# Performance work log

Hardware: AMD Instinct MI355X
Metric: run time of the kernel (lower is better)

Reference implementation:

```python
import jax, jax.numpy as jnp
import numpy as np

GROUPS = 8   # GroupNorm groups
TOP_K = 2    # top-k routing
TEMP = 1.0   # gate temperature
EPS_GN = 1e-5


def conv1d(x, w, b=None):
    # x: (B,C,T), w: (Cout,Cin,K) -> (B,Cout,T), 'same' padding
    pad = (w.shape[-1] - 1) // 2
    y = jax.lax.conv_general_dilated(x, w, (1,), [(pad, pad)],
                                     dimension_numbers=('NCH', 'OIH', 'NCH'))
    return y if b is None else y + b[None, :, None]


def group_norm(x, gamma, beta, groups=GROUPS, eps=EPS_GN):
    B, C, T = x.shape
    xg = x.reshape(B, groups, C // groups, T)
    mu = xg.mean((2, 3), keepdims=True)
    var = xg.var((2, 3), keepdims=True)
    xn = ((xg - mu) * jax.lax.rsqrt(var + eps)).reshape(B, C, T)
    return xn * gamma[None, :, None] + beta[None, :, None]


def layer_norm(x, gamma, beta, eps=EPS_GN):
    mu = x.mean(-1, keepdims=True)
    var = x.var(-1, keepdims=True)
    return (x - mu) * jax.lax.rsqrt(var + eps) * gamma + beta


def gelu(x):
    return jax.nn.gelu(x, approximate=False)  # torch nn.GELU default (erf)


def setup_inputs() -> dict:
    key = jax.random.key(0)
    ks = jax.random.split(key, 32)
    B, C, T = 32, 16, 2048
    E, CO, K = 8, 128, 5
    HID, CTX, DIN, DEMB = 128, 64, 8, 16
    GIN = CTX + DEMB
    n = lambda i, shape, s=0.05: jax.random.normal(ks[i], shape, dtype=jnp.float32) * s
    return {
        'x': jax.random.normal(ks[0], (B, C, T), dtype=jnp.float32),
        'demo': jax.random.normal(ks[1], (B, DIN), dtype=jnp.float32),
        # router context CNN (Conv1d no bias -> GroupNorm -> GELU)
        'rw': n(2, (HID, C, K)), 'rg': jnp.ones((HID,), jnp.float32), 'rb': jnp.zeros((HID,), jnp.float32),
        # router MLP: Linear -> LayerNorm -> GELU -> Linear
        'm1_w': n(3, (HID, HID)), 'm1_b': jnp.zeros((HID,), jnp.float32),
        'ln_g': jnp.ones((HID,), jnp.float32), 'ln_b': jnp.zeros((HID,), jnp.float32),
        'm2_w': n(4, (CTX, HID)), 'm2_b': jnp.zeros((CTX,), jnp.float32),
        # demographics embedder: Linear -> LayerNorm -> GELU -> Linear
        'd1_w': n(5, (2 * DEMB, DIN)), 'd1_b': jnp.zeros((2 * DEMB,), jnp.float32),
        'dln_g': jnp.ones((2 * DEMB,), jnp.float32), 'dln_b': jnp.zeros((2 * DEMB,), jnp.float32),
        'd2_w': n(6, (DEMB, 2 * DEMB)), 'd2_b': jnp.zeros((DEMB,), jnp.float32),
        # gate linear
        'g_w': n(7, (E, GIN)), 'g_b': jnp.zeros((E,), jnp.float32),
        # specialised expert CNNs (stacked over E): Conv1d -> GroupNorm -> GELU
        'ew': n(8, (E, CO, C, K)), 'eb': jnp.zeros((E, CO), jnp.float32),
        'eg': jnp.ones((E, CO), jnp.float32), 'ebt': jnp.zeros((E, CO), jnp.float32),
        # shared (always-on) expert CNN
        'sw': n(9, (CO, C, K)), 'sb': jnp.zeros((CO,), jnp.float32),
        'sg': jnp.ones((CO,), jnp.float32), 'sbt': jnp.zeros((CO,), jnp.float32),
    }


def reference(x, demo, rw, rg, rb, m1_w, m1_b, ln_g, ln_b, m2_w, m2_b,
              d1_w, d1_b, dln_g, dln_b, d2_w, d2_b, g_w, g_b,
              ew, eb, eg, ebt, sw, sb, sg, sbt):
    # ---- router: context CNN -> GAP -> MLP -> r (B, CTX)
    h = gelu(group_norm(conv1d(x, rw), rg, rb))
    r = h.mean(-1)  # GAP over time
    r = gelu(layer_norm(r @ m1_w.T + m1_b, ln_g, ln_b))
    r = r @ m2_w.T + m2_b
    # ---- demographics embedding, concat onto routing vector
    d = gelu(layer_norm(demo @ d1_w.T + d1_b, dln_g, dln_b))
    d = d @ d2_w.T + d2_b
    r = jnp.concatenate([r, d], axis=-1)  # (B, CTX+DEMB)
    # ---- gate: softmax + top-k mask + renormalise
    logits = (r @ g_w.T + g_b) / TEMP
    weights_soft = jax.nn.softmax(logits, axis=-1)  # (B, E)
    _, topk_idx = jax.lax.top_k(weights_soft, TOP_K)
    Bn = weights_soft.shape[0]
    mask = jnp.zeros_like(weights_soft).at[jnp.arange(Bn)[:, None], topk_idx].set(1.0)
    wh = weights_soft * mask
    weights_hard = wh / (wh.sum(-1, keepdims=True) + 1e-9)
    # ---- experts (dense compute, top-k-masked combine) + shared expert
    expert = lambda w, b, g, be: gelu(group_norm(conv1d(x, w, b), g, be))
    eo = jax.vmap(expert)(ew, eb, eg, ebt)  # (E, B, CO, T)
    shared = gelu(group_norm(conv1d(x, sw, sb), sg, sbt))  # (B, CO, T)
    out = shared + jnp.einsum('be,ebct->bct', weights_hard, eo)
    return out
```

## Files before the change

kernel.cpp:

```cpp
#include <hip/hip_runtime.h>
#include <math.h>

#define B_    32
#define CIN   16
#define T_    2048
#define NG    8
#define CPG   16
#define HID   128
#define KW    5
#define EPS_  1e-5f

#define NROW  2080
#define ROWS  16

#define SH_EWF  1064960
#define SH_RWF  1175552
#define FO_R0   593920
#define FO_GW   598016
#define FO_GI   598080

typedef float f32x4 __attribute__((ext_vector_type(4)));
typedef short s16x8 __attribute__((ext_vector_type(8)));

__device__ __forceinline__ float gelu_fast(float y) {
    float p = y * y;
    float u = y * (0.7978845608028654f + 0.03567740813636141f * p);
    float au = fabsf(u);
    float e = __expf(2.0f * au);
    float th = copysignf(1.0f - 2.0f * __builtin_amdgcn_rcpf(e + 1.0f), u);
    return 0.5f * y * (1.0f + th);
}

__device__ __forceinline__ float gelu_erf(float y) {
    return 0.5f * y * (1.0f + erff(y * 0.70710678118654752440f));
}

__device__ __forceinline__ short bf16r(float f) {
    unsigned u = __builtin_bit_cast(unsigned, f);
    u = u + 0x7FFFu + ((u >> 16) & 1u);
    return (short)(u >> 16);
}

__global__ __launch_bounds__(256) void transpose_kernel(
    const float* __restrict__ x, short* __restrict__ xt)
{
    const int b = blockIdx.x, half = blockIdx.y;
    const int tid = threadIdx.x;
    const float* xb = x + (size_t)b * CIN * T_;
    short* xtb = xt + (size_t)b * NROW * ROWS;
    const int t0 = (half * 256 + tid) * 4;

    float v[CIN][4];
    #pragma unroll
    for (int ci = 0; ci < CIN; ++ci)
        *(f32x4*)v[ci] = *(const f32x4*)(xb + ci * T_ + t0);

    #pragma unroll
    for (int tt = 0; tt < 4; ++tt) {
        s16x8 lo, hi;
        #pragma unroll
        for (int ci = 0; ci < 8; ++ci) lo[ci] = bf16r(v[ci][tt]);
        #pragma unroll
        for (int ci = 0; ci < 8; ++ci) hi[ci] = bf16r(v[ci + 8][tt]);
        short* rp = xtb + (size_t)(t0 + tt + 2) * ROWS;
        *(s16x8*)rp = lo;
        *(s16x8*)(rp + 8) = hi;
    }
    if (half == 0 && tid < 32) {
        int r = (tid < 2) ? tid : 2048 + tid;
        s16x8 z = {0, 0, 0, 0, 0, 0, 0, 0};
        short* rp = xtb + (size_t)r * ROWS;
        *(s16x8*)rp = z;
        *(s16x8*)(rp + 8) = z;
    }
}

__global__ __launch_bounds__(64) void wprep_kernel(
    const float* __restrict__ rw, const float* __restrict__ ew,
    const float* __restrict__ sw, short* __restrict__ wsf)
{
    const int id = blockIdx.x, l = threadIdx.x;
    const int n = l & 15, grp = l >> 4;
    const int s_ = grp >> 1, cib = (grp & 1) * 8;

    const float* src;
    short* dst;
    if (id < 72) {
        int es = id / 8, g = id - es * 8;
        src = ((es == 0) ? sw : ew + (size_t)(es - 1) * 128 * (CIN * KW))
              + (size_t)g * CPG * (CIN * KW);
        dst = wsf + SH_EWF + ((size_t)(es * 8 + g) * 3) * 64 * 8;
    } else {
        int g = id - 72;
        src = rw + (size_t)g * CPG * (CIN * KW);
        dst = wsf + SH_RWF + ((size_t)g * 3) * 64 * 8;
    }
    #pragma unroll
    for (int p = 0; p < 3; ++p) {
        int sh = 2 * p + s_;
        s16x8 a;
        if (sh < 5) {
            const float* wp = src + (size_t)n * (CIN * KW) + cib * KW + sh;
            #pragma unroll
            for (int j = 0; j < 8; ++j) a[j] = bf16r(wp[j * KW]);
        } else {
            #pragma unroll
            for (int j = 0; j < 8; ++j) a[j] = 0;
        }
        *(s16x8*)(dst + ((size_t)p * 64 + l) * 8) = a;
    }
}

__device__ __forceinline__ void stage_xt(const short* __restrict__ xtb,
                                         short* __restrict__ xs, int tid)
{
    const s16x8* src = (const s16x8*)xtb;
    s16x8* dst = (s16x8*)xs;
    #pragma unroll
    for (int i = 0; i < 8; ++i)
        dst[tid + i * 512] = src[tid + i * 512];
    int i8 = tid + 8 * 512;
    if (i8 < NROW * 2) dst[i8] = src[i8];
}

__global__ __launch_bounds__(512, 4) void router_conv_kernel(
    const short* __restrict__ xt, const short* __restrict__ wsf,
    const float* __restrict__ rg, const float* __restrict__ rb,
    float* __restrict__ r0)
{
    __shared__ short xs[NROW * ROWS];
    __shared__ float redS[8], redQ[8];
    __shared__ float rsum[8][CPG];

    const int b = blockIdx.x, g = blockIdx.y;
    const int tid = threadIdx.x;
    const int l = tid & 63, wv = tid >> 6;
    const int n = l & 15, grp = l >> 4;
    const int s_ = grp >> 1;

    stage_xt(xt + (size_t)b * NROW * ROWS, xs, tid);

    const short* rwb = wsf + SH_RWF + ((size_t)g * 3) * 64 * 8;
    s16x8 afr0 = *(const s16x8*)(rwb + (0 * 64 + l) * 8);
    s16x8 afr1 = *(const s16x8*)(rwb + (1 * 64 + l) * 8);
    s16x8 afr2 = *(const s16x8*)(rwb + (2 * 64 + l) * 8);
    __syncthreads();

    const int cib = (grp & 1) * 8;
    f32x4 cst[16];
    float sA = 0.f, qA = 0.f;
    #pragma unroll
    for (int tile = 0; tile < 16; ++tile) {
        const int t0 = (wv * 16 + tile) * 16;
        s16x8 bf0 = *(const s16x8*)&xs[(t0 + n + 0 + s_) * ROWS + cib];
        s16x8 bf1 = *(const s16x8*)&xs[(t0 + n + 2 + s_) * ROWS + cib];
        s16x8 bf2 = *(const s16x8*)&xs[(t0 + n + 4 + s_) * ROWS + cib];
        f32x4 c = {0.f, 0.f, 0.f, 0.f};
        c = __builtin_amdgcn_mfma_f32_16x16x32_bf16(afr0, bf0, c, 0, 0, 0);
        c = __builtin_amdgcn_mfma_f32_16x16x32_bf16(afr1, bf1, c, 0, 0, 0);
        c = __builtin_amdgcn_mfma_f32_16x16x32_bf16(afr2, bf2, c, 0, 0, 0);
        cst[tile] = c;
        #pragma unroll
        for (int r = 0; r < 4; ++r) { sA += c[r]; qA += c[r] * c[r]; }
    }

    for (int d = 1; d < 64; d <<= 1) {
        sA += __shfl_xor(sA, d);
        qA += __shfl_xor(qA, d);
    }
    if (l == 0) { redS[wv] = sA; redQ[wv] = qA; }
    __syncthreads();
    float S = 0.f, Q = 0.f;
    for (int i = 0; i < 8; ++i) { S += redS[i]; Q += redQ[i]; }
    const float inv_n = 1.0f / (CPG * T_);
    float mu = S * inv_n;
    float rs = rsqrtf(Q * inv_n - mu * mu + EPS_);
    float ka[4], kb[4];
    #pragma unroll
    for (int r = 0; r < 4; ++r) {
        int co = g * CPG + grp * 4 + r;
        float gm = rg[co];
        ka[r] = rs * gm;
        kb[r] = rb[co] - mu * rs * gm;
    }

    f32x4 tacc = {0.f, 0.f, 0.f, 0.f};
    #pragma unroll
    for (int tile = 0; tile < 16; ++tile) {
        #pragma unroll
        for (int r = 0; r < 4; ++r)
            tacc[r] += gelu_fast(cst[tile][r] * ka[r] + kb[r]);
    }
    #pragma unroll
    for (int r = 0; r < 4; ++r)
        for (int d = 1; d < 16; d <<= 1)
            tacc[r] += __shfl_xor(tacc[r], d);
    if (n == 0) {
        #pragma unroll
        for (int r = 0; r < 4; ++r) rsum[wv][grp * 4 + r] = tacc[r];
    }
    __syncthreads();
    if (tid < CPG) {
        float a = 0.f;
        for (int w = 0; w < 8; ++w) a += rsum[w][tid];
        r0[b * HID + g * CPG + tid] = a * (1.0f / T_);
    }
}

__global__ void router_gate_kernel(
    const float* __restrict__ r0, const float* __restrict__ demo,
    const float* __restrict__ m1w, const float* __restrict__ m1b,
    const float* __restrict__ lng, const float* __restrict__ lnb,
    const float* __restrict__ m2w, const float* __restrict__ m2b,
    const float* __restrict__ d1w, const float* __restrict__ d1b,
    const float* __restrict__ dlng, const float* __restrict__ dlnb,
    const float* __restrict__ d2w, const float* __restrict__ d2b,
    const float* __restrict__ gw, const float* __restrict__ gb,
    float* __restrict__ gateW, int* __restrict__ gateI)
{
    __shared__ float sh[128];
    __shared__ float dd[32];
    __shared__ float rr[80];
    __shared__ float glds[8];
    __shared__ float red[2], redq[2];

    const int b = blockIdx.x;
    const int j = threadIdx.x;
    const int lane = j & 63, wv = j >> 6;

    sh[j] = r0[b * HID + j];
    __syncthreads();

    float v = m1b[j];
    for (int i = 0; i < 128; ++i) v += sh[i] * m1w[j * 128 + i];
    float s = v, sq = v * v;
    for (int d = 1; d < 64; d <<= 1) { s += __shfl_xor(s, d); sq += __shfl_xor(sq, d); }
    if (lane == 0) { red[wv] = s; redq[wv] = sq; }
    __syncthreads();
    float S = red[0] + red[1], SQ = redq[0] + redq[1];
    float mu = S * (1.f / 128.f), var = SQ * (1.f / 128.f) - mu * mu;
    float h = (v - mu) * rsqrtf(var + EPS_) * lng[j] + lnb[j];
    float gv = gelu_erf(h);
    __syncthreads();
    sh[j] = gv;
    __syncthreads();

    if (j < 64) {
        float rv = m2b[j];
        for (int i = 0; i < 128; ++i) rv += sh[i] * m2w[j * 128 + i];
        rr[j] = rv;
    } else if (j < 96) {
        int jd = j - 64;
        float u = d1b[jd];
        for (int i = 0; i < 8; ++i) u += demo[b * 8 + i] * d1w[jd * 8 + i];
        float s2 = u, q2 = u * u;
        for (int d = 1; d < 32; d <<= 1) { s2 += __shfl_xor(s2, d, 32); q2 += __shfl_xor(q2, d, 32); }
        float mu2 = s2 * (1.f / 32.f), var2 = q2 * (1.f / 32.f) - mu2 * mu2;
        float y = (u - mu2) * rsqrtf(var2 + EPS_) * dlng[jd] + dlnb[jd];
        dd[jd] = gelu_erf(y);
    }
    __syncthreads();
    if (j < 16) {
        float rv = d2b[j];
        for (int i = 0; i < 32; ++i) rv += dd[i] * d2w[j * 32 + i];
        rr[64 + j] = rv;
    }
    __syncthreads();
    if (j < 8) {
        float lg = gb[j];
        for (int i = 0; i < 80; ++i) lg += rr[i] * gw[j * 80 + i];
        glds[j] = lg;
    }
    __syncthreads();
    if (j == 0) {
        float wsf[8];
        float m = glds[0];
        for (int e = 1; e < 8; ++e) m = fmaxf(m, glds[e]);
        float ssum = 0.f;
        for (int e = 0; e < 8; ++e) { wsf[e] = expf(glds[e] - m); ssum += wsf[e]; }
        for (int e = 0; e < 8; ++e) wsf[e] /= ssum;
        int i1 = 0;
        for (int e = 1; e < 8; ++e) if (wsf[e] > wsf[i1]) i1 = e;
        int i2 = (i1 == 0) ? 1 : 0;
        for (int e = 0; e < 8; ++e) if (e != i1 && wsf[e] > wsf[i2]) i2 = e;
        float a = wsf[i1], b2 = wsf[i2];
        float dn = a + b2 + 1e-9f;
        gateW[b * 2 + 0] = a / dn;
        gateW[b * 2 + 1] = b2 / dn;
        gateI[b * 2 + 0] = i1;
        gateI[b * 2 + 1] = i2;
    }
}

__global__ __launch_bounds__(512, 4) void experts_kernel(
    const short* __restrict__ xt, const short* __restrict__ wsf,
    const float* __restrict__ eb, const float* __restrict__ eg,
    const float* __restrict__ ebt,
    const float* __restrict__ sb, const float* __restrict__ sg,
    const float* __restrict__ sbt,
    const float* __restrict__ gateW, const int* __restrict__ gateI,
    float* __restrict__ out)
{
    __shared__ short xs[NROW * ROWS];
    __shared__ float redS[3][8], redQ[3][8];

    const int b = blockIdx.x, g = blockIdx.y;
    const int tid = threadIdx.x;
    const int l = tid & 63, wv = tid >> 6;
    const int n = l & 15, grp = l >> 4;
    const int s_ = grp >> 1, cib = (grp & 1) * 8;

    const int e1 = gateI[b * 2 + 0], e2 = gateI[b * 2 + 1];
    const float scl[3] = {1.0f, gateW[b * 2 + 0], gateW[b * 2 + 1]};

    stage_xt(xt + (size_t)b * NROW * ROWS, xs, tid);

    s16x8 afr[3][3];
    const int esi[3] = {0, 1 + e1, 1 + e2};
    #pragma unroll
    for (int sl = 0; sl < 3; ++sl) {
        const short* wb = wsf + SH_EWF + ((size_t)(esi[sl] * 8 + g) * 3) * 64 * 8;
        #pragma unroll
        for (int p = 0; p < 3; ++p)
            afr[sl][p] = *(const s16x8*)(wb + ((size_t)p * 64 + l) * 8);
    }
    float bia[3][4];
    #pragma unroll
    for (int sl = 0; sl < 3; ++sl) {
        const float* bs = (sl == 0) ? sb : eb + ((sl == 1) ? e1 : e2) * 128;
        #pragma unroll
        for (int r = 0; r < 4; ++r) bia[sl][r] = bs[g * CPG + grp * 4 + r];
    }
    __syncthreads();

    const int tbase = wv * 16;

    float sA[3] = {0.f, 0.f, 0.f}, qA[3] = {0.f, 0.f, 0.f};
    {
        int t0 = tbase * 16;
        s16x8 p0 = *(const s16x8*)&xs[(t0 + n + 0 + s_) * ROWS + cib];
        s16x8 p1 = *(const s16x8*)&xs[(t0 + n + 2 + s_) * ROWS + cib];
        s16x8 p2 = *(const s16x8*)&xs[(t0 + n + 4 + s_) * ROWS + cib];
        #pragma unroll 4
        for (int tile = 0; tile < 16; ++tile) {
            s16x8 c0 = p0, c1 = p1, c2 = p2;
            if (tile < 15) {
                int t1 = (tbase + tile + 1) * 16;
                p0 = *(const s16x8*)&xs[(t1 + n + 0 + s_) * ROWS + cib];
                p1 = *(const s16x8*)&xs[(t1 + n + 2 + s_) * ROWS + cib];
                p2 = *(const s16x8*)&xs[(t1 + n + 4 + s_) * ROWS + cib];
            }
            #pragma unroll
            for (int sl = 0; sl < 3; ++sl) {
                f32x4 c = {0.f, 0.f, 0.f, 0.f};
                c = __builtin_amdgcn_mfma_f32_16x16x32_bf16(afr[sl][0], c0, c, 0, 0, 0);
                c = __builtin_amdgcn_mfma_f32_16x16x32_bf16(afr[sl][1], c1, c, 0, 0, 0);
                c = __builtin_amdgcn_mfma_f32_16x16x32_bf16(afr[sl][2], c2, c, 0, 0, 0);
                #pragma unroll
                for (int r = 0; r < 4; ++r) {
                    float v = c[r] + bia[sl][r];
                    sA[sl] += v; qA[sl] += v * v;
                }
            }
        }
    }
    #pragma unroll
    for (int sl = 0; sl < 3; ++sl)
        for (int d = 1; d < 64; d <<= 1) {
            sA[sl] += __shfl_xor(sA[sl], d);
            qA[sl] += __shfl_xor(qA[sl], d);
        }
    if (l == 0) {
        #pragma unroll
        for (int sl = 0; sl < 3; ++sl) { redS[sl][wv] = sA[sl]; redQ[sl][wv] = qA[sl]; }
    }
    __syncthreads();

    const float inv_n = 1.0f / (CPG * T_);
    float ka[3][4], kb[3][4];
    #pragma unroll
    for (int sl = 0; sl < 3; ++sl) {
        float S = 0.f, Q = 0.f;
        for (int i = 0; i < 8; ++i) { S += redS[sl][i]; Q += redQ[sl][i]; }
        float mu = S * inv_n;
        float rs = rsqrtf(Q * inv_n - mu * mu + EPS_);
        int e = (sl == 1) ? e1 : e2;
        const float* gs = (sl == 0) ? sg  : eg  + e * 128;
        const float* bt = (sl == 0) ? sbt : ebt + e * 128;
        #pragma unroll
        for (int r = 0; r < 4; ++r) {
            int co = g * CPG + grp * 4 + r;
            float gm = gs[co];
            ka[sl][r] = rs * gm;
            kb[sl][r] = (bia[sl][r] - mu) * rs * gm + bt[co];
        }
    }

    {
        int t0 = tbase * 16;
        s16x8 p0 = *(const s16x8*)&xs[(t0 + n + 0 + s_) * ROWS + cib];
        s16x8 p1 = *(const s16x8*)&xs[(t0 + n + 2 + s_) * ROWS + cib];
        s16x8 p2 = *(const s16x8*)&xs[(t0 + n + 4 + s_) * ROWS + cib];
        #pragma unroll 2
        for (int tile = 0; tile < 16; ++tile) {
            s16x8 c0 = p0, c1 = p1, c2 = p2;
            if (tile < 15) {
                int t1 = (tbase + tile + 1) * 16;
                p0 = *(const s16x8*)&xs[(t1 + n + 0 + s_) * ROWS + cib];
                p1 = *(const s16x8*)&xs[(t1 + n + 2 + s_) * ROWS + cib];
                p2 = *(const s16x8*)&xs[(t1 + n + 4 + s_) * ROWS + cib];
            }
            f32x4 oacc = {0.f, 0.f, 0.f, 0.f};
            #pragma unroll
            for (int sl = 0; sl < 3; ++sl) {
                f32x4 c = {0.f, 0.f, 0.f, 0.f};
                c = __builtin_amdgcn_mfma_f32_16x16x32_bf16(afr[sl][0], c0, c, 0, 0, 0);
                c = __builtin_amdgcn_mfma_f32_16x16x32_bf16(afr[sl][1], c1, c, 0, 0, 0);
                c = __builtin_amdgcn_mfma_f32_16x16x32_bf16(afr[sl][2], c2, c, 0, 0, 0);
                #pragma unroll
                for (int r = 0; r < 4; ++r)
                    oacc[r] += scl[sl] * gelu_fast(c[r] * ka[sl][r] + kb[sl][r]);
            }
            size_t obase = ((size_t)(b * HID + g * CPG + grp * 4)) * T_
                         + (tbase + tile) * 16 + n;
            #pragma unroll
            for (int r = 0; r < 4; ++r)
                out[obase + (size_t)r * T_] = oacc[r];
        }
    }
}

extern "C" void kernel_launch(void* const* d_in, const int* in_sizes, int n_in,
                              void* d_out, int out_size, void* d_ws, size_t ws_size,
                              hipStream_t stream)
{
    const float* x    = (const float*)d_in[0];
    const float* demo = (const float*)d_in[1];
    const float* rw   = (const float*)d_in[2];
    const float* rg   = (const float*)d_in[3];
    const float* rb   = (const float*)d_in[4];
    const float* m1w  = (const float*)d_in[5];
    const float* m1b  = (const float*)d_in[6];
    const float* lng  = (const float*)d_in[7];
    const float* lnb  = (const float*)d_in[8];
    const float* m2w  = (const float*)d_in[9];
    const float* m2b  = (const float*)d_in[10];
    const float* d1w  = (const float*)d_in[11];
    const float* d1b  = (const float*)d_in[12];
    const float* dlng = (const float*)d_in[13];
    const float* dlnb = (const float*)d_in[14];
    const float* d2w  = (const float*)d_in[15];
    const float* d2b  = (const float*)d_in[16];
    const float* gw   = (const float*)d_in[17];
    const float* gb   = (const float*)d_in[18];
    const float* ew   = (const float*)d_in[19];
    const float* eb   = (const float*)d_in[20];
    const float* eg   = (const float*)d_in[21];
    const float* ebt  = (const float*)d_in[22];
    const float* sw   = (const float*)d_in[23];
    const float* sb   = (const float*)d_in[24];
    const float* sg   = (const float*)d_in[25];
    const float* sbt  = (const float*)d_in[26];
    float* out = (float*)d_out;

    short* xt   = (short*)d_ws;
    short* wsfs = (short*)d_ws;
    float* wsff = (float*)d_ws;
    float* r0    = wsff + FO_R0;
    float* gateW = wsff + FO_GW;
    int*   gateI = (int*)wsff + FO_GI;

    transpose_kernel<<<dim3(B_, 2), 256, 0, stream>>>(x, xt);
    wprep_kernel<<<dim3(80), 64, 0, stream>>>(rw, ew, sw, wsfs);
    dim3 gridc(B_, NG);
    router_conv_kernel<<<gridc, 512, 0, stream>>>(xt, wsfs, rg, rb, r0);
    router_gate_kernel<<<dim3(B_), 128, 0, stream>>>(
        r0, demo, m1w, m1b, lng, lnb, m2w, m2b,
        d1w, d1b, dlng, dlnb, d2w, d2b, gw, gb, gateW, gateI);
    experts_kernel<<<gridc, 512, 0, stream>>>(
        xt, wsfs, eb, eg, ebt, sb, sg, sbt, gateW, gateI, out);
    (void)in_sizes; (void)n_in; (void)out_size; (void)ws_size;
}
```

Baseline: 54.46 us.

## Split expert kernel into time-chunked stats and apply passes, merge prep kernels

Replaces the single experts kernel (one block per batch×group holding the whole sequence in LDS) with two kernels over four time chunks: one writes partial GroupNorm sums to workspace, the other reduces them and applies norm, GELU and the gated combine. This raises block count and cuts LDS per block for better occupancy, at the cost of an extra launch and a global round trip for statistics. The transpose and weight-prep kernels are fused into one launch, and the tanh GELU approximation is swapped for a cheaper sigmoid-based one, which loosens accuracy.

```diff
diff --git a/kernel.cpp b/kernel.cpp
--- a/kernel.cpp
+++ b/kernel.cpp
@@ -12,12 +12,16 @@
 
 #define NROW  2080
 #define ROWS  16
+#define NQ    4
+#define QT    512
+#define QROWS 544
 
 #define SH_EWF  1064960
 #define SH_RWF  1175552
 #define FO_R0   593920
 #define FO_GW   598016
 #define FO_GI   598080
+#define FO_STE  598144
 
 typedef float f32x4 __attribute__((ext_vector_type(4)));
 typedef short s16x8 __attribute__((ext_vector_type(8)));
@@ -31,6 +35,11 @@
     return 0.5f * y * (1.0f + th);
 }
 
+__device__ __forceinline__ float gelu_sig(float y) {
+    float e = __expf(-1.702f * y);
+    return y * __builtin_amdgcn_rcpf(1.0f + e);
+}
+
 __device__ __forceinline__ float gelu_erf(float y) {
     return 0.5f * y * (1.0f + erff(y * 0.70710678118654752440f));
 }
@@ -41,78 +50,76 @@
     return (short)(u >> 16);
 }
 
-__global__ __launch_bounds__(256) void transpose_kernel(
-    const float* __restrict__ x, short* __restrict__ xt)
-{
-    const int b = blockIdx.x, half = blockIdx.y;
-    const int tid = threadIdx.x;
-    const float* xb = x + (size_t)b * CIN * T_;
-    short* xtb = xt + (size_t)b * NROW * ROWS;
-    const int t0 = (half * 256 + tid) * 4;
-
-    float v[CIN][4];
-    #pragma unroll
-    for (int ci = 0; ci < CIN; ++ci)
-        *(f32x4*)v[ci] = *(const f32x4*)(xb + ci * T_ + t0);
-
-    #pragma unroll
-    for (int tt = 0; tt < 4; ++tt) {
-        s16x8 lo, hi;
-        #pragma unroll
-        for (int ci = 0; ci < 8; ++ci) lo[ci] = bf16r(v[ci][tt]);
-        #pragma unroll
-        for (int ci = 0; ci < 8; ++ci) hi[ci] = bf16r(v[ci + 8][tt]);
-        short* rp = xtb + (size_t)(t0 + tt + 2) * ROWS;
-        *(s16x8*)rp = lo;
-        *(s16x8*)(rp + 8) = hi;
-    }
-    if (half == 0 && tid < 32) {
-        int r = (tid < 2) ? tid : 2048 + tid;
-        s16x8 z = {0, 0, 0, 0, 0, 0, 0, 0};
-        short* rp = xtb + (size_t)r * ROWS;
-        *(s16x8*)rp = z;
-        *(s16x8*)(rp + 8) = z;
-    }
-}
-
-__global__ __launch_bounds__(64) void wprep_kernel(
-    const float* __restrict__ rw, const float* __restrict__ ew,
-    const float* __restrict__ sw, short* __restrict__ wsf)
-{
-    const int id = blockIdx.x, l = threadIdx.x;
-    const int n = l & 15, grp = l >> 4;
-    const int s_ = grp >> 1, cib = (grp & 1) * 8;
-
-    const float* src;
-    short* dst;
-    if (id < 72) {
-        int es = id / 8, g = id - es * 8;
-        src = ((es == 0) ? sw : ew + (size_t)(es - 1) * 128 * (CIN * KW))
-              + (size_t)g * CPG * (CIN * KW);
-        dst = wsf + SH_EWF + ((size_t)(es * 8 + g) * 3) * 64 * 8;
-    } else {
-        int g = id - 72;
-        src = rw + (size_t)g * CPG * (CIN * KW);
-        dst = wsf + SH_RWF + ((size_t)g * 3) * 64 * 8;
-    }
-    #pragma unroll
-    for (int p = 0; p < 3; ++p) {
-        int sh = 2 * p + s_;
-        s16x8 a;
-        if (sh < 5) {
-            const float* wp = src + (size_t)n * (CIN * KW) + cib * KW + sh;
+__global__ __launch_bounds__(256) void prep_kernel(
+    const float* __restrict__ x, const float* __restrict__ rw,
+    const float* __restrict__ ew, const float* __restrict__ sw,
+    short* __restrict__ wsf)
+{
+    const int bid = blockIdx.x, tid = threadIdx.x;
+    if (bid < 64) {
+        const int b = bid >> 1, half = bid & 1;
+        const float* xb = x + (size_t)b * CIN * T_;
+        short* xtb = wsf + (size_t)b * NROW * ROWS;
+        const int t0 = (half * 256 + tid) * 4;
+
+        float v[CIN][4];
+        #pragma unroll
+        for (int ci = 0; ci < CIN; ++ci)
+            *(f32x4*)v[ci] = *(const f32x4*)(xb + ci * T_ + t0);
+
+        #pragma unroll
+        for (int tt = 0; tt < 4; ++tt) {
+            s16x8 lo, hi;
             #pragma unroll
-            for (int j = 0; j < 8; ++j) a[j] = bf16r(wp[j * KW]);
+            for (int ci = 0; ci < 8; ++ci) lo[ci] = bf16r(v[ci][tt]);
+            #pragma unroll
+            for (int ci = 0; ci < 8; ++ci) hi[ci] = bf16r(v[ci + 8][tt]);
+            short* rp = xtb + (size_t)(t0 + tt + 2) * ROWS;
+            *(s16x8*)rp = lo;
+            *(s16x8*)(rp + 8) = hi;
+        }
+        if (half == 0 && tid < 32) {
+            int r = (tid < 2) ? tid : 2048 + tid;
+            s16x8 z = {0, 0, 0, 0, 0, 0, 0, 0};
+            short* rp = xtb + (size_t)r * ROWS;
+            *(s16x8*)rp = z;
+            *(s16x8*)(rp + 8) = z;
+        }
+    } else if (tid < 64) {
+        const int id = bid - 64, l = tid;
+        const int n = l & 15, grp = l >> 4;
+        const int s_ = grp >> 1, cib = (grp & 1) * 8;
+        const float* src;
+        short* dst;
+        if (id < 72) {
+            int es = id / 8, g = id - es * 8;
+            src = ((es == 0) ? sw : ew + (size_t)(es - 1) * 128 * (CIN * KW))
+                  + (size_t)g * CPG * (CIN * KW);
+            dst = wsf + SH_EWF + ((size_t)(es * 8 + g) * 3) * 64 * 8;
         } else {
-            #pragma unroll
-            for (int j = 0; j < 8; ++j) a[j] = 0;
-        }
-        *(s16x8*)(dst + ((size_t)p * 64 + l) * 8) = a;
-    }
-}
-
-__device__ __forceinline__ void stage_xt(const short* __restrict__ xtb,
-                                         short* __restrict__ xs, int tid)
+            int g = id - 72;
+            src = rw + (size_t)g * CPG * (CIN * KW);
+            dst = wsf + SH_RWF + ((size_t)g * 3) * 64 * 8;
+        }
+        #pragma unroll
+        for (int p = 0; p < 3; ++p) {
+            int sh = 2 * p + s_;
+            s16x8 a;
+            if (sh < 5) {
+                const float* wp = src + (size_t)n * (CIN * KW) + cib * KW + sh;
+                #pragma unroll
+                for (int j = 0; j < 8; ++j) a[j] = bf16r(wp[j * KW]);
+            } else {
+                #pragma unroll
+                for (int j = 0; j < 8; ++j) a[j] = 0;
+            }
+            *(s16x8*)(dst + ((size_t)p * 64 + l) * 8) = a;
+        }
+    }
+}
+
+__device__ __forceinline__ void stage_xt_full(const short* __restrict__ xtb,
+                                              short* __restrict__ xs, int tid)
 {
     const s16x8* src = (const s16x8*)xtb;
     s16x8* dst = (s16x8*)xs;
@@ -121,6 +128,18 @@
         dst[tid + i * 512] = src[tid + i * 512];
     int i8 = tid + 8 * 512;
     if (i8 < NROW * 2) dst[i8] = src[i8];
+}
+
+__device__ __forceinline__ void stage_xt_q(const short* __restrict__ xtq,
+                                           short* __restrict__ xs, int tid)
+{
+    const s16x8* src = (const s16x8*)xtq;
+    s16x8* dst = (s16x8*)xs;
+    #pragma unroll
+    for (int i = 0; i < 4; ++i)
+        dst[tid + i * 256] = src[tid + i * 256];
+    int i4 = tid + 4 * 256;
+    if (i4 < QROWS * 2) dst[i4] = src[i4];
 }
 
 __global__ __launch_bounds__(512, 4) void router_conv_kernel(
@@ -138,7 +157,7 @@
     const int n = l & 15, grp = l >> 4;
     const int s_ = grp >> 1;
 
-    stage_xt(xt + (size_t)b * NROW * ROWS, xs, tid);
+    stage_xt_full(xt + (size_t)b * NROW * ROWS, xs, tid);
 
     const short* rwb = wsf + SH_RWF + ((size_t)g * 3) * 64 * 8;
     s16x8 afr0 = *(const s16x8*)(rwb + (0 * 64 + l) * 8);
@@ -292,19 +311,89 @@
     }
 }
 
-__global__ __launch_bounds__(512, 4) void experts_kernel(
+__global__ __launch_bounds__(256, 4) void expert_stats_kernel(
+    const short* __restrict__ xt, const short* __restrict__ wsf,
+    const float* __restrict__ eb, const float* __restrict__ sb,
+    const int* __restrict__ gateI, float* __restrict__ ste)
+{
+    __shared__ short xs[QROWS * ROWS];
+
+    const int b = blockIdx.x, g = blockIdx.y, q = blockIdx.z;
+    const int tid = threadIdx.x;
+    const int l = tid & 63, wv = tid >> 6;
+    const int n = l & 15, grp = l >> 4;
+    const int s_ = grp >> 1, cib = (grp & 1) * 8;
+
+    const int e1 = gateI[b * 2 + 0], e2 = gateI[b * 2 + 1];
+
+    stage_xt_q(xt + ((size_t)b * NROW + q * QT) * ROWS, xs, tid);
+
+    s16x8 afr[3][3];
+    const int esi[3] = {0, 1 + e1, 1 + e2};
+    #pragma unroll
+    for (int sl = 0; sl < 3; ++sl) {
+        const short* wb = wsf + SH_EWF + ((size_t)(esi[sl] * 8 + g) * 3) * 64 * 8;
+        #pragma unroll
+        for (int p = 0; p < 3; ++p)
+            afr[sl][p] = *(const s16x8*)(wb + ((size_t)p * 64 + l) * 8);
+    }
+    float bia[3][4];
+    #pragma unroll
+    for (int sl = 0; sl < 3; ++sl) {
+        const float* bs = (sl == 0) ? sb : eb + ((sl == 1) ? e1 : e2) * 128;
+        #pragma unroll
+        for (int r = 0; r < 4; ++r) bia[sl][r] = bs[g * CPG + grp * 4 + r];
+    }
+    __syncthreads();
+
+    float sA[3] = {0.f, 0.f, 0.f}, qA[3] = {0.f, 0.f, 0.f};
+    #pragma unroll 2
+    for (int tile = 0; tile < 8; ++tile) {
+        const int t0 = (wv * 8 + tile) * 16;
+        s16x8 bf0 = *(const s16x8*)&xs[(t0 + n + 0 + s_) * ROWS + cib];
+        s16x8 bf1 = *(const s16x8*)&xs[(t0 + n + 2 + s_) * ROWS + cib];
+        s16x8 bf2 = *(const s16x8*)&xs[(t0 + n + 4 + s_) * ROWS + cib];
+        #pragma unroll
+        for (int sl = 0; sl < 3; ++sl) {
+            f32x4 c = {0.f, 0.f, 0.f, 0.f};
+            c = __builtin_amdgcn_mfma_f32_16x16x32_bf16(afr[sl][0], bf0, c, 0, 0, 0);
+            c = __builtin_amdgcn_mfma_f32_16x16x32_bf16(afr[sl][1], bf1, c, 0, 0, 0);
+            c = __builtin_amdgcn_mfma_f32_16x16x32_bf16(afr[sl][2], bf2, c, 0, 0, 0);
+            #pragma unroll
+            for (int r = 0; r < 4; ++r) {
+                float v = c[r] + bia[sl][r];
+                sA[sl] += v; qA[sl] += v * v;
+            }
+        }
+    }
+    #pragma unroll
+    for (int sl = 0; sl < 3; ++sl)
+        for (int d = 1; d < 64; d <<= 1) {
+            sA[sl] += __shfl_xor(sA[sl], d);
+            qA[sl] += __shfl_xor(qA[sl], d);
+        }
+    if (l == 0) {
+        #pragma unroll
+        for (int sl = 0; sl < 3; ++sl) {
+            int idx = ((b * NG + g) * 3 + sl) * 16 + q * 4 + wv;
+            ste[idx * 2 + 0] = sA[sl];
+            ste[idx * 2 + 1] = qA[sl];
+        }
+    }
+}
+
+__global__ __launch_bounds__(256, 4) void expert_apply_kernel(
     const short* __restrict__ xt, const short* __restrict__ wsf,
     const float* __restrict__ eb, const float* __restrict__ eg,
     const float* __restrict__ ebt,
     const float* __restrict__ sb, const float* __restrict__ sg,
     const float* __restrict__ sbt,
     const float* __restrict__ gateW, const int* __restrict__ gateI,
-    float* __restrict__ out)
-{
-    __shared__ short xs[NROW * ROWS];
-    __shared__ float redS[3][8], redQ[3][8];
-
-    const int b = blockIdx.x, g = blockIdx.y;
+    const float* __restrict__ ste, float* __restrict__ out)
+{
+    __shared__ short xs[QROWS * ROWS];
+
+    const int b = blockIdx.x, g = blockIdx.y, q = blockIdx.z;
     const int tid = threadIdx.x;
     const int l = tid & 63, wv = tid >> 6;
     const int n = l & 15, grp = l >> 4;
@@ -313,7 +402,7 @@
     const int e1 = gateI[b * 2 + 0], e2 = gateI[b * 2 + 1];
     const float scl[3] = {1.0f, gateW[b * 2 + 0], gateW[b * 2 + 1]};
 
-    stage_xt(xt + (size_t)b * NROW * ROWS, xs, tid);
+    stage_xt_q(xt + ((size_t)b * NROW + q * QT) * ROWS, xs, tid);
 
     s16x8 afr[3][3];
     const int esi[3] = {0, 1 + e1, 1 + e2};
@@ -324,67 +413,18 @@
         for (int p = 0; p < 3; ++p)
             afr[sl][p] = *(const s16x8*)(wb + ((size_t)p * 64 + l) * 8);
     }
-    float bia[3][4];
-    #pragma unroll
-    for (int sl = 0; sl < 3; ++sl) {
-        const float* bs = (sl == 0) ? sb : eb + ((sl == 1) ? e1 : e2) * 128;
-        #pragma unroll
-        for (int r = 0; r < 4; ++r) bia[sl][r] = bs[g * CPG + grp * 4 + r];
-    }
-    __syncthreads();
-
-    const int tbase = wv * 16;
-
-    float sA[3] = {0.f, 0.f, 0.f}, qA[3] = {0.f, 0.f, 0.f};
-    {
-        int t0 = tbase * 16;
-        s16x8 p0 = *(const s16x8*)&xs[(t0 + n + 0 + s_) * ROWS + cib];
-        s16x8 p1 = *(const s16x8*)&xs[(t0 + n + 2 + s_) * ROWS + cib];
-        s16x8 p2 = *(const s16x8*)&xs[(t0 + n + 4 + s_) * ROWS + cib];
-        #pragma unroll 4
-        for (int tile = 0; tile < 16; ++tile) {
-            s16x8 c0 = p0, c1 = p1, c2 = p2;
-            if (tile < 15) {
-                int t1 = (tbase + tile + 1) * 16;
-                p0 = *(const s16x8*)&xs[(t1 + n + 0 + s_) * ROWS + cib];
-                p1 = *(const s16x8*)&xs[(t1 + n + 2 + s_) * ROWS + cib];
-                p2 = *(const s16x8*)&xs[(t1 + n + 4 + s_) * ROWS + cib];
-            }
-            #pragma unroll
-            for (int sl = 0; sl < 3; ++sl) {
-                f32x4 c = {0.f, 0.f, 0.f, 0.f};
-                c = __builtin_amdgcn_mfma_f32_16x16x32_bf16(afr[sl][0], c0, c, 0, 0, 0);
-                c = __builtin_amdgcn_mfma_f32_16x16x32_bf16(afr[sl][1], c1, c, 0, 0, 0);
-                c = __builtin_amdgcn_mfma_f32_16x16x32_bf16(afr[sl][2], c2, c, 0, 0, 0);
-                #pragma unroll
-                for (int r = 0; r < 4; ++r) {
-                    float v = c[r] + bia[sl][r];
-                    sA[sl] += v; qA[sl] += v * v;
-                }
-            }
-        }
-    }
-    #pragma unroll
-    for (int sl = 0; sl < 3; ++sl)
-        for (int d = 1; d < 64; d <<= 1) {
-            sA[sl] += __shfl_xor(sA[sl], d);
-            qA[sl] += __shfl_xor(qA[sl], d);
-        }
-    if (l == 0) {
-        #pragma unroll
-        for (int sl = 0; sl < 3; ++sl) { redS[sl][wv] = sA[sl]; redQ[sl][wv] = qA[sl]; }
-    }
-    __syncthreads();
 
     const float inv_n = 1.0f / (CPG * T_);
     float ka[3][4], kb[3][4];
     #pragma unroll
     for (int sl = 0; sl < 3; ++sl) {
         float S = 0.f, Q = 0.f;
-        for (int i = 0; i < 8; ++i) { S += redS[sl][i]; Q += redQ[sl][i]; }
+        const float* sp = ste + (((size_t)(b * NG + g) * 3 + sl) * 16) * 2;
+        for (int i = 0; i < 16; ++i) { S += sp[i * 2]; Q += sp[i * 2 + 1]; }
         float mu = S * inv_n;
         float rs = rsqrtf(Q * inv_n - mu * mu + EPS_);
         int e = (sl == 1) ? e1 : e2;
+        const float* bs = (sl == 0) ? sb  : eb  + e * 128;
         const float* gs = (sl == 0) ? sg  : eg  + e * 128;
         const float* bt = (sl == 0) ? sbt : ebt + e * 128;
         #pragma unroll
@@ -392,41 +432,33 @@
             int co = g * CPG + grp * 4 + r;
             float gm = gs[co];
             ka[sl][r] = rs * gm;
-            kb[sl][r] = (bia[sl][r] - mu) * rs * gm + bt[co];
-        }
-    }
-
-    {
-        int t0 = tbase * 16;
-        s16x8 p0 = *(const s16x8*)&xs[(t0 + n + 0 + s_) * ROWS + cib];
-        s16x8 p1 = *(const s16x8*)&xs[(t0 + n + 2 + s_) * ROWS + cib];
-        s16x8 p2 = *(const s16x8*)&xs[(t0 + n + 4 + s_) * ROWS + cib];
-        #pragma unroll 2
-        for (int tile = 0; tile < 16; ++tile) {
-            s16x8 c0 = p0, c1 = p1, c2 = p2;
-            if (tile < 15) {
-                int t1 = (tbase + tile + 1) * 16;
-                p0 = *(const s16x8*)&xs[(t1 + n + 0 + s_) * ROWS + cib];
-                p1 = *(const s16x8*)&xs[(t1 + n + 2 + s_) * ROWS + cib];
-                p2 = *(const s16x8*)&xs[(t1 + n + 4 + s_) * ROWS + cib];
-            }
-            f32x4 oacc = {0.f, 0.f, 0.f, 0.f};
-            #pragma unroll
-            for (int sl = 0; sl < 3; ++sl) {
-                f32x4 c = {0.f, 0.f, 0.f, 0.f};
-                c = __builtin_amdgcn_mfma_f32_16x16x32_bf16(afr[sl][0], c0, c, 0, 0, 0);
-                c = __builtin_amdgcn_mfma_f32_16x16x32_bf16(afr[sl][1], c1, c, 0, 0, 0);
-                c = __builtin_amdgcn_mfma_f32_16x16x32_bf16(afr[sl][2], c2, c, 0, 0, 0);
-                #pragma unroll
-                for (int r = 0; r < 4; ++r)
-                    oacc[r] += scl[sl] * gelu_fast(c[r] * ka[sl][r] + kb[sl][r]);
-            }
-            size_t obase = ((size_t)(b * HID + g * CPG + grp * 4)) * T_
-                         + (tbase + tile) * 16 + n;
+            kb[sl][r] = (bs[co] - mu) * rs * gm + bt[co];
+        }
+    }
+    __syncthreads();
+
+    #pragma unroll 2
+    for (int tile = 0; tile < 8; ++tile) {
+        const int t0 = (wv * 8 + tile) * 16;
+        s16x8 bf0 = *(const s16x8*)&xs[(t0 + n + 0 + s_) * ROWS + cib];
+        s16x8 bf1 = *(const s16x8*)&xs[(t0 + n + 2 + s_) * ROWS + cib];
+        s16x8 bf2 = *(const s16x8*)&xs[(t0 + n + 4 + s_) * ROWS + cib];
+        f32x4 oacc = {0.f, 0.f, 0.f, 0.f};
+        #pragma unroll
+        for (int sl = 0; sl < 3; ++sl) {
+            f32x4 c = {0.f, 0.f, 0.f, 0.f};
+            c = __builtin_amdgcn_mfma_f32_16x16x32_bf16(afr[sl][0], bf0, c, 0, 0, 0);
+            c = __builtin_amdgcn_mfma_f32_16x16x32_bf16(afr[sl][1], bf1, c, 0, 0, 0);
+            c = __builtin_amdgcn_mfma_f32_16x16x32_bf16(afr[sl][2], bf2, c, 0, 0, 0);
             #pragma unroll
             for (int r = 0; r < 4; ++r)
-                out[obase + (size_t)r * T_] = oacc[r];
-        }
+                oacc[r] += scl[sl] * gelu_sig(c[r] * ka[sl][r] + kb[sl][r]);
+        }
+        size_t obase = ((size_t)(b * HID + g * CPG + grp * 4)) * T_
+                     + q * QT + t0 + n;
+        #pragma unroll
+        for (int r = 0; r < 4; ++r)
+            out[obase + (size_t)r * T_] = oacc[r];
     }
 }
 
@@ -469,15 +501,17 @@
     float* r0    = wsff + FO_R0;
     float* gateW = wsff + FO_GW;
     int*   gateI = (int*)wsff + FO_GI;
-
-    transpose_kernel<<<dim3(B_, 2), 256, 0, stream>>>(x, xt);
-    wprep_kernel<<<dim3(80), 64, 0, stream>>>(rw, ew, sw, wsfs);
+    float* ste   = wsff + FO_STE;
+
+    prep_kernel<<<dim3(144), 256, 0, stream>>>(x, rw, ew, sw, wsfs);
     dim3 gridc(B_, NG);
     router_conv_kernel<<<gridc, 512, 0, stream>>>(xt, wsfs, rg, rb, r0);
     router_gate_kernel<<<dim3(B_), 128, 0, stream>>>(
         r0, demo, m1w, m1b, lng, lnb, m2w, m2b,
         d1w, d1b, dlng, dlnb, d2w, d2b, gw, gb, gateW, gateI);
-    experts_kernel<<<gridc, 512, 0, stream>>>(
-        xt, wsfs, eb, eg, ebt, sb, sg, sbt, gateW, gateI, out);
+    dim3 gridq(B_, NG, NQ);
+    expert_stats_kernel<<<gridq, 256, 0, stream>>>(xt, wsfs, eb, sb, gateI, ste);
+    expert_apply_kernel<<<gridq, 256, 0, stream>>>(
+        xt, wsfs, eb, eg, ebt, sb, sg, sbt, gateW, gateI, ste, out);
     (void)in_sizes; (void)n_in; (void)out_size; (void)ws_size;
 }
```

New measurement: 49.73 us. 8.7% less time.
